# Performance work log

Hardware: AMD Instinct MI355X
Metric: run time of the kernel (lower is better)

The kernel has to match this reference:

```python
import jax, jax.numpy as jnp
from jax import lax
import numpy as np

# (pad, pool_kernel(h,w), pool_stride(h,w)) for each of the 7 conv layers
_CONV_CFG = [
    (1, (2, 2), (2, 2)),
    (1, (2, 2), (2, 2)),
    (1, (2, 2), (2, 1)),
    (1, (2, 2), (2, 1)),
    (1, (2, 2), (2, 2)),
    (1, (2, 2), (2, 1)),
    (0, (1, 1), (1, 1)),
]


def _conv_layer(x, w, b, pad, pool_k, pool_s):
    y = lax.conv_general_dilated(x, w, (1, 1), [(pad, pad), (pad, pad)],
                                 dimension_numbers=("NCHW", "OIHW", "NCHW"))
    y = jax.nn.relu(y + b[None, :, None, None])
    if pool_k != (1, 1):
        y = lax.reduce_window(y, -jnp.inf, lax.max, (1, 1) + pool_k, (1, 1) + pool_s, "VALID")
    return y


def _lstm_dir(x, wih, whh, bih, bhh, reverse):
    # x: [B,T,I]; PyTorch gate order i,f,g,o
    B = x.shape[0]
    H = whh.shape[1]
    xg = jnp.einsum("bti,gi->btg", x, wih) + bih + bhh  # [B,T,4H]

    def step(carry, xt):
        h, c = carry
        g = xt + h @ whh.T
        i, f, gg, o = jnp.split(g, 4, axis=-1)
        c = jax.nn.sigmoid(f) * c + jax.nn.sigmoid(i) * jnp.tanh(gg)
        h = jax.nn.sigmoid(o) * jnp.tanh(c)
        return (h, c), h

    init = (jnp.zeros((B, H), x.dtype), jnp.zeros((B, H), x.dtype))
    _, hs = lax.scan(step, init, jnp.swapaxes(xg, 0, 1), reverse=reverse)
    return jnp.swapaxes(hs, 0, 1)  # [B,T,H], time-ordered for both directions


def _bilstm2(x, wih, whh, bih, bhh, base):
    # 2-layer bidirectional LSTM; weight slots base..base+3 = (l0_fwd,l0_bwd,l1_fwd,l1_bwd)
    for l in range(2):
        i0 = base + 2 * l
        fwd = _lstm_dir(x, wih[i0], whh[i0], bih[i0], bhh[i0], False)
        bwd = _lstm_dir(x, wih[i0 + 1], whh[i0 + 1], bih[i0 + 1], bhh[i0 + 1], True)
        x = jnp.concatenate([fwd, bwd], axis=-1)
    return x


def _forward(x, conv_w0, conv_b0, conv_w1, conv_b1, conv_w2, conv_b2, conv_w3, conv_b3,
             conv_w4, conv_b4, conv_w5, conv_b5, conv_w6, conv_b6,
             lstm_wih, lstm_whh, lstm_bih, lstm_bhh,
             enc_proj_w, enc_proj_b, dec_proj_w, dec_proj_b, v_w,
             dec_wih, dec_whh, dec_bih, dec_bhh, dense_w, dense_b):
    conv_w = [conv_w0, conv_w1, conv_w2, conv_w3, conv_w4, conv_w5, conv_w6]
    conv_b = [conv_b0, conv_b1, conv_b2, conv_b3, conv_b4, conv_b5, conv_b6]
    y = x
    for i, (pad, pk, ps) in enumerate(_CONV_CFG):
        y = _conv_layer(y, conv_w[i], conv_b[i], pad, pk, ps)
    # y: [B,512,1,T] -> squeeze height, put time first-major: [B,T,512]
    y = jnp.transpose(y[:, :, 0, :], (0, 2, 1))
    seq = _bilstm2(y, lstm_wih, lstm_whh, lstm_bih, lstm_bhh, 0)
    seq = _bilstm2(seq, lstm_wih, lstm_whh, lstm_bih, lstm_bhh, 4)  # [B,T,512]

    # additive attention: enc projection is h-independent, precompute once
    enc = jnp.einsum("bte,ae->bta", seq, enc_proj_w) + enc_proj_b  # [B,T,256]
    B = x.shape[0]

    def dec_step(carry, _):
        h, c = carry
        dec = h @ dec_proj_w.T + dec_proj_b                      # [B,256]
        scores = jnp.tanh(enc + dec[:, None, :]) @ v_w[0]        # [B,T]
        aw = jax.nn.softmax(scores, axis=1)
        ctx = jnp.einsum("bt,bte->be", aw, seq)                  # [B,512]
        g = ctx @ dec_wih.T + dec_bih + h @ dec_whh.T + dec_bhh  # [B,2048]
        i, f, gg, o = jnp.split(g, 4, axis=-1)
        c = jax.nn.sigmoid(f) * c + jax.nn.sigmoid(i) * jnp.tanh(gg)
        h = jax.nn.sigmoid(o) * jnp.tanh(c)
        return (h, c), h @ dense_w.T + dense_b

    init = (jnp.zeros((B, 512), x.dtype), jnp.zeros((B, 512), x.dtype))
    _, outs = lax.scan(dec_step, init, None, length=25)  # [25,B,99] == permute(1,0,2)
    return outs


def setup_inputs() -> dict:
    key = jax.random.key(0)
    ks = jax.random.split(key, 32)

    def rn(i, shape, std):
        return jax.random.normal(ks[i], shape, jnp.float32) * std

    d = {"x": jax.random.normal(ks[0], (16, 1, 128, 512), jnp.float32)}
    chans = [(1, 64, 3), (64, 128, 3), (128, 256, 3), (256, 512, 3),
             (512, 512, 3), (512, 512, 3), (512, 512, 2)]
    for i, (ci, co, k) in enumerate(chans):
        d[f"conv_w{i}"] = rn(1 + i, (co, ci, k, k), (2.0 / (ci * k * k)) ** 0.5)
        d[f"conv_b{i}"] = rn(8 + i, (co,), 0.02)
    d["lstm_wih"] = rn(15, (8, 1024, 512), 0.06)
    d["lstm_whh"] = rn(16, (8, 1024, 256), 0.06)
    d["lstm_bih"] = rn(17, (8, 1024), 0.06)
    d["lstm_bhh"] = rn(18, (8, 1024), 0.06)
    d["enc_proj_w"] = rn(19, (256, 512), 0.04)
    d["enc_proj_b"] = rn(20, (256,), 0.02)
    d["dec_proj_w"] = rn(21, (256, 512), 0.04)
    d["dec_proj_b"] = rn(22, (256,), 0.02)
    d["v_w"] = rn(23, (1, 256), 0.06)
    d["dec_wih"] = rn(24, (2048, 512), 0.04)
    d["dec_whh"] = rn(25, (2048, 512), 0.04)
    d["dec_bih"] = rn(26, (2048,), 0.02)
    d["dec_bhh"] = rn(27, (2048,), 0.02)
    d["dense_w"] = rn(28, (99, 512), 0.04)
    d["dense_b"] = rn(29, (99,), 0.02)
    return d


def reference(x, conv_w0, conv_b0, conv_w1, conv_b1, conv_w2, conv_b2, conv_w3, conv_b3,
              conv_w4, conv_b4, conv_w5, conv_b5, conv_w6, conv_b6,
              lstm_wih, lstm_whh, lstm_bih, lstm_bhh,
              enc_proj_w, enc_proj_b, dec_proj_w, dec_proj_b, v_w,
              dec_wih, dec_whh, dec_bih, dec_bhh, dense_w, dense_b):
    return _forward(x, conv_w0, conv_b0, conv_w1, conv_b1, conv_w2, conv_b2, conv_w3, conv_b3,
                    conv_w4, conv_b4, conv_w5, conv_b5, conv_w6, conv_b6,
                    lstm_wih, lstm_whh, lstm_bih, lstm_bhh,
                    enc_proj_w, enc_proj_b, dec_proj_w, dec_proj_b, v_w,
                    dec_wih, dec_whh, dec_bih, dec_bhh, dense_w, dense_b)
```

## Files before the change

### kernel.cpp

```cpp
#include <hip/hip_runtime.h>
#include <math.h>

typedef short bf16x8 __attribute__((ext_vector_type(8)));
typedef float f32x4  __attribute__((ext_vector_type(4)));

__device__ __forceinline__ float sigmf(float x){ return 1.f/(1.f+expf(-x)); }
__device__ __forceinline__ short f2bf(float f){
    unsigned u = __float_as_uint(f);
    u = (u + 0x7FFFu + ((u>>16)&1u)) >> 16;
    return (short)u;
}
__device__ __forceinline__ float bf2f(short s){
    return __uint_as_float(((unsigned)(unsigned short)s) << 16);
}

__global__ void wsplit(const float* __restrict__ w, short* __restrict__ whi, short* __restrict__ wlo,
                       int Cout, int Cin, int KW, int total)
{
    int idx = blockIdx.x*256 + threadIdx.x;
    if (idx >= total) return;
    int l = idx & 63; int t = idx >> 6;
    int KST = Cin >> 5;
    int ks = t % KST; t /= KST;
    int nCoQ = Cout >> 4;
    int coQ = t % nCoQ; int kk = t / nCoQ;
    int ky = kk / KW, kx = kk % KW;
    int co = coQ*16 + (l & 15);
    int ci = ks*32 + (l >> 4)*8;
    bf16x8 h, lo;
#pragma unroll
    for (int e = 0; e < 8; ++e) {
        float wv = w[(((size_t)co*Cin + ci + e)*KW + ky)*KW + kx];
        short hb = f2bf(wv);
        h[e] = hb;
        lo[e] = f2bf(wv - bf2f(hb));
    }
    ((bf16x8*)whi)[idx] = h;
    ((bf16x8*)wlo)[idx] = lo;
}

template<int KW, int PKH, int PKW, int PSW, int PAD, bool FUSE0>
__launch_bounds__(256)
__global__ void conv_mfma(const float* __restrict__ in, const short* __restrict__ wm,
                          const float* __restrict__ bias, float* __restrict__ out,
                          int Cin, int H, int W, int Cout, int Hp, int Wp, int Wel,
                          const float* __restrict__ w0, const float* __restrict__ b0)
{
    constexpr int TAPS = KW*KW;
    constexpr int SR   = PKH + KW - 1;
    constexpr int XT   = 64;
    constexpr int XTH  = 67;
    constexpr int POB  = (XT - PKW)/PSW + 1;
    __shared__ union {
        short s[2][16][XTH][8];
        float y[64][132];
    } u;
    __shared__ float w0s[640];

    const int tid  = threadIdx.x;
    const int lane = tid & 63;
    const int wid  = tid >> 6;
    const int l15  = lane & 15, l4 = lane >> 4;
    const int nCoT = Cout >> 7;
    const int b    = blockIdx.z / nCoT;
    const int ct   = blockIdx.z % nCoT;
    const int co_blk = ct << 7;
    const int hp   = blockIdx.y;
    const int px0  = blockIdx.x * POB;
    const int x0   = px0 * PSW;
    const int y0   = hp * PKH;
    const int cow  = wid >> 1;
    const int xw   = (wid & 1) * 32;
    const int KST  = Cin >> 5;
    const int nCoQ = Cout >> 4;

    if constexpr (FUSE0) {
        for (int i = tid; i < 640; i += 256) w0s[i] = (i < 576) ? w0[i] : b0[i-576];
    }

    f32x4 acc[4][2][PKH];
#pragma unroll
    for (int c = 0; c < 4; ++c)
#pragma unroll
        for (int xf = 0; xf < 2; ++xf)
#pragma unroll
            for (int r = 0; r < PKH; ++r) acc[c][xf][r] = (f32x4){0.f,0.f,0.f,0.f};

    const float* inb = FUSE0 ? (in + (size_t)b*128*512) : (in + (size_t)b*H*W*Cin);

    for (int ci0 = 0; ci0 < Cin; ci0 += 32) {
        __syncthreads();
        constexpr int ITEMS = SR*XTH*4;
        for (int it = tid; it < ITEMS; it += 256) {
            int kslot = it & 3;
            int x  = (it >> 2) % XTH;
            int r  = (it >> 2) / XTH;
            int y  = y0 - PAD + r;
            int xg = x0 - PAD + x;
            float v[8];
            if constexpr (FUSE0) {
                if (y >= 0 && y < H && xg >= 0 && xg < W) {
                    float xin[4][4];
                    int iy0 = 2*y - 1, ix0 = 2*xg - 1;
#pragma unroll
                    for (int dy = 0; dy < 4; ++dy) {
                        int iy = iy0 + dy;
                        bool oky = (iy >= 0) && (iy < 128);
#pragma unroll
                        for (int dx = 0; dx < 4; ++dx) {
                            int ix = ix0 + dx;
                            xin[dy][dx] = (oky && ix >= 0 && ix < 512) ? inb[(size_t)iy*512 + ix] : 0.f;
                        }
                    }
#pragma unroll
                    for (int c = 0; c < 8; ++c) {
                        int co = ci0 + kslot*8 + c;
                        const float* w9 = &w0s[co*9];
                        float p00=0.f,p01=0.f,p10=0.f,p11=0.f;
#pragma unroll
                        for (int ky = 0; ky < 3; ++ky)
#pragma unroll
                            for (int kx = 0; kx < 3; ++kx) {
                                float wv = w9[ky*3+kx];
                                p00 = fmaf(xin[ky  ][kx  ], wv, p00);
                                p01 = fmaf(xin[ky  ][kx+1], wv, p01);
                                p10 = fmaf(xin[ky+1][kx  ], wv, p10);
                                p11 = fmaf(xin[ky+1][kx+1], wv, p11);
                            }
                        float m = fmaxf(fmaxf(p00,p01), fmaxf(p10,p11)) + w0s[576+co];
                        v[c] = fmaxf(m, 0.f);
                    }
                } else {
#pragma unroll
                    for (int c = 0; c < 8; ++c) v[c] = 0.f;
                }
            } else {
                if (y >= 0 && y < H && xg >= 0 && xg < W) {
                    const float* p = inb + ((size_t)y*W + xg)*Cin + ci0 + kslot*8;
                    float4 a = *(const float4*)p;
                    float4 bq = *(const float4*)(p+4);
                    v[0]=a.x; v[1]=a.y; v[2]=a.z; v[3]=a.w;
                    v[4]=bq.x; v[5]=bq.y; v[6]=bq.z; v[7]=bq.w;
                } else {
#pragma unroll
                    for (int c = 0; c < 8; ++c) v[c] = 0.f;
                }
            }
            bf16x8 h8, l8;
#pragma unroll
            for (int c = 0; c < 8; ++c) {
                short hb = f2bf(v[c]);
                h8[c] = hb;
                l8[c] = f2bf(v[c] - bf2f(hb));
            }
            *(bf16x8*)&u.s[0][r*4+kslot][x][0] = h8;
            *(bf16x8*)&u.s[1][r*4+kslot][x][0] = l8;
        }
        __syncthreads();

        const int ks = ci0 >> 5;
        for (int kk = 0; kk < TAPS; ++kk) {
            const int ky = kk / KW, kx = kk % KW;
            bf16x8 ah[4], al[4];
            const size_t abase = (((size_t)kk*nCoQ + (co_blk>>4) + cow*4)*KST + ks)*512 + lane*8;
            const size_t cstr  = (size_t)KST*512;
#pragma unroll
            for (int c = 0; c < 4; ++c) {
                ah[c] = *(const bf16x8*)(wm + abase + c*cstr);
                al[c] = *(const bf16x8*)(wm + Wel + abase + c*cstr);
            }
#pragma unroll
            for (int r = 0; r < PKH; ++r) {
                const int sr = r + ky;
                bf16x8 bh[2], bl[2];
#pragma unroll
                for (int xf = 0; xf < 2; ++xf) {
                    int xcol = xw + xf*16 + l15 + kx;
                    bh[xf] = *(const bf16x8*)&u.s[0][sr*4 + l4][xcol][0];
                    bl[xf] = *(const bf16x8*)&u.s[1][sr*4 + l4][xcol][0];
                }
#pragma unroll
                for (int c = 0; c < 4; ++c)
#pragma unroll
                    for (int xf = 0; xf < 2; ++xf) {
                        acc[c][xf][r] = __builtin_amdgcn_mfma_f32_16x16x32_bf16(ah[c], bh[xf], acc[c][xf][r], 0,0,0);
                        acc[c][xf][r] = __builtin_amdgcn_mfma_f32_16x16x32_bf16(ah[c], bl[xf], acc[c][xf][r], 0,0,0);
                        acc[c][xf][r] = __builtin_amdgcn_mfma_f32_16x16x32_bf16(al[c], bh[xf], acc[c][xf][r], 0,0,0);
                    }
            }
        }
    }

    __syncthreads();
#pragma unroll
    for (int c = 0; c < 4; ++c) {
        int co_l = cow*64 + c*16 + l4*4;
        float4 b4 = *(const float4*)&bias[co_blk + co_l];
#pragma unroll
        for (int xf = 0; xf < 2; ++xf) {
            f32x4 v = acc[c][xf][0];
            if (PKH == 2) {
                f32x4 v1 = acc[c][xf][1];
                v[0]=fmaxf(v[0],v1[0]); v[1]=fmaxf(v[1],v1[1]);
                v[2]=fmaxf(v[2],v1[2]); v[3]=fmaxf(v[3],v1[3]);
            }
            v[0]+=b4.x; v[1]+=b4.y; v[2]+=b4.z; v[3]+=b4.w;
            int x = xw + xf*16 + l15;
            *(f32x4*)&u.y[x][co_l] = v;
        }
    }
    __syncthreads();
    for (int i = tid; i < POB*128; i += 256) {
        int co = i & 127, p = i >> 7;
        int x = p * PSW;
        float v = u.y[x][co];
        if (PKW == 2) v = fmaxf(v, u.y[x+1][co]);
        v = fmaxf(v, 0.f);
        int px = px0 + p;
        if (px < Wp)
            out[(((size_t)b*Hp + hp)*Wp + px)*Cout + co_blk + co] = v;
    }
}

__launch_bounds__(256)
__global__ void gemm_nt(const float* __restrict__ A, const float* __restrict__ Bm,
                        const float* __restrict__ bias1, const float* __restrict__ bias2,
                        float* __restrict__ C, int M, int N, int K)
{
    __shared__ float As[16][68];
    __shared__ float Bs[16][68];
    const int tid = threadIdx.x;
    const int tx = tid & 15, ty = tid >> 4;
    const int row0 = blockIdx.y*64, col0 = blockIdx.x*64;
    float acc[4][4] = {};
    for (int k0 = 0; k0 < K; k0 += 16) {
#pragma unroll
        for (int i = 0; i < 4; ++i) {
            int e  = tid + i*256;
            int r  = e >> 4, kk = e & 15;
            int gr = row0 + r, gk = k0 + kk;
            As[kk][r] = (gr < M) ? A[(size_t)gr*K + gk] : 0.f;
            int gc = col0 + r;
            Bs[kk][r] = (gc < N) ? Bm[(size_t)gc*K + gk] : 0.f;
        }
        __syncthreads();
#pragma unroll
        for (int kk = 0; kk < 16; ++kk) {
            float av[4], bv[4];
#pragma unroll
            for (int i=0;i<4;++i) av[i] = As[kk][ty*4+i];
#pragma unroll
            for (int j=0;j<4;++j) bv[j] = Bs[kk][tx*4+j];
#pragma unroll
            for (int i=0;i<4;++i)
#pragma unroll
                for (int j=0;j<4;++j) acc[i][j] = fmaf(av[i], bv[j], acc[i][j]);
        }
        __syncthreads();
    }
#pragma unroll
    for (int i=0;i<4;++i)
#pragma unroll
        for (int j=0;j<4;++j) {
            int r = row0 + ty*4 + i, cc = col0 + tx*4 + j;
            if (r < M && cc < N) {
                float v = acc[i][j];
                if (bias1) v += bias1[cc];
                if (bias2) v += bias2[cc];
                C[(size_t)r*N + cc] = v;
            }
        }
}

__global__ void transpose2d(const float* __restrict__ in, float* __restrict__ out, int R, int C)
{
    int idx = blockIdx.x*256 + threadIdx.x;
    if (idx >= R*C) return;
    int r = idx / C, c = idx % C;
    out[(size_t)c*R + r] = in[idx];
}

__global__ void transpose_whh4(const float* __restrict__ in, float* __restrict__ out)
{
    int idx = blockIdx.x*256 + threadIdx.x;
    if (idx >= 8*1024*256) return;
    int l = idx / 262144, rem = idx % 262144;
    int g = rem >> 8, k = rem & 255;
    int j = g & 255, gate = g >> 8;
    out[(size_t)l*262144 + ((size_t)k*256 + j)*4 + gate] = in[idx];
}

__global__ void transpose_w4(const float* __restrict__ in, float* __restrict__ out)
{
    int idx = blockIdx.x*256 + threadIdx.x;
    if (idx >= 2048*512) return;
    int row = idx >> 9, k = idx & 511;
    int gate = row >> 9, j = row & 511;
    out[((size_t)k*512 + j)*4 + gate] = in[idx];
}

__launch_bounds__(1024)
__global__ void lstm_scan2(const float* __restrict__ xgf, const float* __restrict__ xgb,
                           const float* __restrict__ w4f, const float* __restrict__ w4b,
                           float* __restrict__ hout, int T)
{
    __shared__ float hs[256];
    __shared__ float part[4][256][4];
    const int b = blockIdx.x, dir = blockIdx.y;
    const int tid = threadIdx.x;
    const int j = tid & 255, ks = tid >> 8;
    const float* xg = dir ? xgb : xgf;
    const float4* w4 = (const float4*)(dir ? w4b : w4f);
    float c = 0.f;
    if (ks == 0) hs[j] = 0.f;
    __syncthreads();
    float* outp = hout + dir*256 + j;
    for (int s = 0; s < T; ++s) {
        int t = dir ? (T-1-s) : s;
        float a0=0.f,a1=0.f,a2=0.f,a3=0.f;
        const float4* wp = w4 + (size_t)(ks*64)*256 + j;
#pragma unroll 8
        for (int kk = 0; kk < 64; ++kk) {
            float hv = hs[ks*64 + kk];
            float4 w = wp[(size_t)kk*256];
            a0 = fmaf(hv, w.x, a0); a1 = fmaf(hv, w.y, a1);
            a2 = fmaf(hv, w.z, a2); a3 = fmaf(hv, w.w, a3);
        }
        part[ks][j][0]=a0; part[ks][j][1]=a1; part[ks][j][2]=a2; part[ks][j][3]=a3;
        __syncthreads();
        if (ks == 0) {
            const float* xr = xg + ((size_t)b*T + t)*1024;
            float gi = xr[j]     + part[0][j][0]+part[1][j][0]+part[2][j][0]+part[3][j][0];
            float gf = xr[256+j] + part[0][j][1]+part[1][j][1]+part[2][j][1]+part[3][j][1];
            float gg = xr[512+j] + part[0][j][2]+part[1][j][2]+part[2][j][2]+part[3][j][2];
            float go = xr[768+j] + part[0][j][3]+part[1][j][3]+part[2][j][3]+part[3][j][3];
            c = sigmf(gf)*c + sigmf(gi)*tanhf(gg);
            float h = sigmf(go)*tanhf(c);
            hs[j] = h;
            outp[((size_t)b*T + t)*512] = h;
        }
        __syncthreads();
    }
}

__global__ void zero_hc(float* __restrict__ h, float* __restrict__ c)
{
    int i = blockIdx.x*256 + threadIdx.x;
    if (i < 16*512) { h[i] = 0.f; c[i] = 0.f; }
}

__launch_bounds__(256)
__global__ void dec_att(const float* __restrict__ h, const float* __restrict__ seq,
                        const float* __restrict__ enc, const float* __restrict__ dpwT,
                        const float* __restrict__ dpb, const float* __restrict__ vw,
                        float* __restrict__ ctx, int T)
{
    __shared__ float hsm[512], dec[256], sc[64];
    const int b = blockIdx.x, tid = threadIdx.x;
    hsm[tid]     = h[b*512 + tid];
    hsm[256+tid] = h[b*512 + 256 + tid];
    __syncthreads();
    float s = dpb[tid];
    for (int k = 0; k < 512; ++k) s = fmaf(hsm[k], dpwT[(size_t)k*256 + tid], s);
    dec[tid] = s;
    __syncthreads();
    {
        int t = tid >> 2, sub = tid & 3;
        float p = 0.f;
        if (t < T) {
            const float* er = enc + ((size_t)b*T + t)*256 + sub*64;
            const float* dc = dec + sub*64;
            const float* vv = vw + sub*64;
            for (int a = 0; a < 64; ++a) p = fmaf(tanhf(er[a] + dc[a]), vv[a], p);
        }
        p += __shfl_xor(p, 1, 4); p += __shfl_xor(p, 2, 4);
        if (t < T && sub == 0) sc[t] = p;
    }
    __syncthreads();
    if (tid < 64) {
        float v = (tid < T) ? sc[tid] : -1e30f;
        float m = v;
        for (int o = 1; o < 64; o <<= 1) m = fmaxf(m, __shfl_xor(m, o, 64));
        float e = (tid < T) ? expf(v - m) : 0.f;
        float ssum = e;
        for (int o = 1; o < 64; o <<= 1) ssum += __shfl_xor(ssum, o, 64);
        if (tid < T) sc[tid] = e / ssum;
    }
    __syncthreads();
#pragma unroll
    for (int half = 0; half < 2; ++half) {
        int col = tid + half*256;
        float acc = 0.f;
        const float* sr = seq + (size_t)b*T*512 + col;
        for (int t = 0; t < T; ++t) acc = fmaf(sc[t], sr[(size_t)t*512], acc);
        ctx[b*512 + col] = acc;
    }
}

__launch_bounds__(256)
__global__ void gates_part(const float* __restrict__ ctx, const float* __restrict__ h,
                           const float* __restrict__ wi4, const float* __restrict__ wh4,
                           float* __restrict__ gpart)
{
    __shared__ float xs[16][128], hsh[16][128];
    const int jt = blockIdx.x, ks = blockIdx.y;
    const int tid = threadIdx.x;
    const int jl = tid & 127, bh = tid >> 7;
    const int j = jt*128 + jl;
    const int k0 = ks*128;
    for (int idx = tid; idx < 2048; idx += 256) {
        int bb = idx >> 7, kk = idx & 127;
        xs[bb][kk]  = ctx[bb*512 + k0 + kk];
        hsh[bb][kk] = h[bb*512 + k0 + kk];
    }
    __syncthreads();
    float acc[8][4];
#pragma unroll
    for (int bi=0;bi<8;++bi)
#pragma unroll
        for (int g=0;g<4;++g) acc[bi][g]=0.f;
    const float4* wip = (const float4*)wi4 + (size_t)k0*512 + j;
    const float4* whp = (const float4*)wh4 + (size_t)k0*512 + j;
#pragma unroll 2
    for (int kk = 0; kk < 128; ++kk) {
        float4 wa = wip[(size_t)kk*512];
        float4 wb = whp[(size_t)kk*512];
#pragma unroll
        for (int bi = 0; bi < 8; ++bi) {
            int bb = bh*8 + bi;
            float xv = xs[bb][kk], hv = hsh[bb][kk];
            acc[bi][0] = fmaf(xv, wa.x, fmaf(hv, wb.x, acc[bi][0]));
            acc[bi][1] = fmaf(xv, wa.y, fmaf(hv, wb.y, acc[bi][1]));
            acc[bi][2] = fmaf(xv, wa.z, fmaf(hv, wb.z, acc[bi][2]));
            acc[bi][3] = fmaf(xv, wa.w, fmaf(hv, wb.w, acc[bi][3]));
        }
    }
    float* gp = gpart + (size_t)ks*16*2048;
#pragma unroll
    for (int bi = 0; bi < 8; ++bi)
#pragma unroll
        for (int g = 0; g < 4; ++g)
            gp[(size_t)(bh*8+bi)*2048 + j*4 + g] = acc[bi][g];
}

__launch_bounds__(512)
__global__ void cell_dense(float* __restrict__ h, float* __restrict__ c,
                           const float* __restrict__ gpart,
                           const float* __restrict__ bih, const float* __restrict__ bhh,
                           const float* __restrict__ dwT, const float* __restrict__ dnb,
                           float* __restrict__ out)
{
    __shared__ float hsh[512];
    const int b = blockIdx.x, j = threadIdx.x;
    float gi = bih[j]        + bhh[j];
    float gf = bih[512+j]    + bhh[512+j];
    float gg = bih[1024+j]   + bhh[1024+j];
    float go = bih[1536+j]   + bhh[1536+j];
#pragma unroll
    for (int ks = 0; ks < 4; ++ks) {
        float4 gp = *(const float4*)(gpart + (size_t)ks*16*2048 + (size_t)b*2048 + j*4);
        gi += gp.x; gf += gp.y; gg += gp.z; go += gp.w;
    }
    float cn = sigmf(gf)*c[b*512+j] + sigmf(gi)*tanhf(gg);
    float hn = sigmf(go)*tanhf(cn);
    c[b*512+j] = cn; h[b*512+j] = hn; hsh[j] = hn;
    __syncthreads();
    int o = j >> 2, sub = j & 3;
    float p = 0.f;
    if (o < 99) {
        const float* hk = hsh + sub*128;
        const float* wk = dwT + (size_t)sub*128*99 + o;
        for (int k = 0; k < 128; ++k) p = fmaf(hk[k], wk[(size_t)k*99], p);
    }
    p += __shfl_xor(p, 1, 4); p += __shfl_xor(p, 2, 4);
    if (o < 99 && sub == 0) out[b*99 + o] = p + dnb[o];
}

extern "C" void kernel_launch(void* const* d_in, const int* in_sizes, int n_in,
                              void* d_out, int out_size, void* d_ws, size_t ws_size,
                              hipStream_t stream)
{
    (void)in_sizes; (void)n_in; (void)out_size; (void)ws_size;
    const float* x = (const float*)d_in[0];
    const float* convw[7]; const float* convb[7];
    for (int i = 0; i < 7; ++i) { convw[i] = (const float*)d_in[1+2*i]; convb[i] = (const float*)d_in[2+2*i]; }
    const float* lw   = (const float*)d_in[15];
    const float* lr   = (const float*)d_in[16];
    const float* lbi  = (const float*)d_in[17];
    const float* lbh  = (const float*)d_in[18];
    const float* encW = (const float*)d_in[19];
    const float* encB = (const float*)d_in[20];
    const float* dpw  = (const float*)d_in[21];
    const float* dpb  = (const float*)d_in[22];
    const float* vw   = (const float*)d_in[23];
    const float* dwih = (const float*)d_in[24];
    const float* dwhh = (const float*)d_in[25];
    const float* dbih = (const float*)d_in[26];
    const float* dbhh = (const float*)d_in[27];
    const float* dnw  = (const float*)d_in[28];
    const float* dnb  = (const float*)d_in[29];
    float* outp = (float*)d_out;

    float* ws    = (float*)d_ws;
    float* bufA  = ws;
    float* bufB  = ws + 8388608;
    float* wscr  = ws + 16777216;
    float* S0    = ws + 19136512;
    float* SY    = ws + 19636224;
    float* xg_f  = ws + 20135936;
    float* xg_b  = ws + 21135360;
    float* whhT4 = ws + 22134784;
    float* encb  = ws + 24231936;
    float* dpwT  = ws + 24481792;
    float* dwT   = ws + 24612864;
    float* hbuf  = ws + 24663552;
    float* cbuf  = ws + 24671744;
    float* ctxb  = ws + 24679936;
    float* gpart = ws + 24688128;
    float* wihT4 = bufA;
    float* whh2T4= bufB;

    short* whi = (short*)wscr;

    {
        int Wel = 9*(128/16)*(64/32)*512;
        wsplit<<<(Wel/8+255)/256, 256, 0, stream>>>(convw[1], whi, whi+Wel, 128, 64, 3, Wel/8);
        conv_mfma<3,2,2,2,1,true><<<dim3(4,32,16), 256, 0, stream>>>(
            x, whi, convb[1], bufA, 64,64,256,128, 32,128, Wel, convw[0], convb[0]);
    }
    {
        int Wel = 9*(256/16)*(128/32)*512;
        wsplit<<<(Wel/8+255)/256, 256, 0, stream>>>(convw[2], whi, whi+Wel, 256, 128, 3, Wel/8);
        conv_mfma<3,2,2,1,1,false><<<dim3(3,16,32), 256, 0, stream>>>(
            bufA, whi, convb[2], bufB, 128,32,128,256, 16,127, Wel, nullptr, nullptr);
    }
    {
        int Wel = 9*(512/16)*(256/32)*512;
        wsplit<<<(Wel/8+255)/256, 256, 0, stream>>>(convw[3], whi, whi+Wel, 512, 256, 3, Wel/8);
        conv_mfma<3,2,2,1,1,false><<<dim3(2,8,64), 256, 0, stream>>>(
            bufB, whi, convb[3], bufA, 256,16,127,512, 8,126, Wel, nullptr, nullptr);
    }
    {
        int Wel = 9*(512/16)*(512/32)*512;
        wsplit<<<(Wel/8+255)/256, 256, 0, stream>>>(convw[4], whi, whi+Wel, 512, 512, 3, Wel/8);
        conv_mfma<3,2,2,2,1,false><<<dim3(2,4,64), 256, 0, stream>>>(
            bufA, whi, convb[4], bufB, 512,8,126,512, 4,63, Wel, nullptr, nullptr);
    }
    {
        int Wel = 9*(512/16)*(512/32)*512;
        wsplit<<<(Wel/8+255)/256, 256, 0, stream>>>(convw[5], whi, whi+Wel, 512, 512, 3, Wel/8);
        conv_mfma<3,2,2,1,1,false><<<dim3(1,2,64), 256, 0, stream>>>(
            bufB, whi, convb[5], bufA, 512,4,63,512, 2,62, Wel, nullptr, nullptr);
    }
    {
        int Wel = 4*(512/16)*(512/32)*512;
        wsplit<<<(Wel/8+255)/256, 256, 0, stream>>>(convw[6], whi, whi+Wel, 512, 512, 2, Wel/8);
        conv_mfma<2,1,1,1,0,false><<<dim3(1,1,64), 256, 0, stream>>>(
            bufA, whi, convb[6], S0, 512,2,62,512, 1,61, Wel, nullptr, nullptr);
    }

    transpose_whh4<<<(8*1024*256 + 255)/256, 256, 0, stream>>>(lr, whhT4);
    transpose2d<<<(256*512 + 255)/256, 256, 0, stream>>>(dpw, dpwT, 256, 512);
    transpose_w4<<<(2048*512 + 255)/256, 256, 0, stream>>>(dwih, wihT4);
    transpose_w4<<<(2048*512 + 255)/256, 256, 0, stream>>>(dwhh, whh2T4);
    transpose2d<<<(99*512 + 255)/256, 256, 0, stream>>>(dnw, dwT, 99, 512);

    const int T = 61, M = 16*T;
    float* cur = S0; float* nxt = SY;
    for (int L = 0; L < 4; ++L) {
        int s0 = 2*L;
        gemm_nt<<<dim3(16, (M+63)/64), 256, 0, stream>>>(cur, lw + (size_t)s0*1024*512,
            lbi + s0*1024, lbh + s0*1024, xg_f, M, 1024, 512);
        gemm_nt<<<dim3(16, (M+63)/64), 256, 0, stream>>>(cur, lw + (size_t)(s0+1)*1024*512,
            lbi + (s0+1)*1024, lbh + (s0+1)*1024, xg_b, M, 1024, 512);
        lstm_scan2<<<dim3(16,2), 1024, 0, stream>>>(xg_f, xg_b,
            whhT4 + (size_t)s0*262144, whhT4 + (size_t)(s0+1)*262144, nxt, T);
        float* tmp = cur; cur = nxt; nxt = tmp;
    }

    gemm_nt<<<dim3(4, (M+63)/64), 256, 0, stream>>>(cur, encW, encB, nullptr, encb, M, 256, 512);

    zero_hc<<<32, 256, 0, stream>>>(hbuf, cbuf);
    for (int step = 0; step < 25; ++step) {
        dec_att<<<16, 256, 0, stream>>>(hbuf, cur, encb, dpwT, dpb, vw, ctxb, T);
        gates_part<<<dim3(4,4), 256, 0, stream>>>(ctxb, hbuf, wihT4, whh2T4, gpart);
        cell_dense<<<16, 512, 0, stream>>>(hbuf, cbuf, gpart, dbih, dbhh, dwT, dnb,
                                           outp + (size_t)step*16*99);
    }
}
```

Before: 5.371 ms.

## Use split-bf16 MFMA for LSTM input GEMMs and bf16 recurrent weights

Replaces the two fp32 SIMT input-projection GEMMs per LSTM layer with a single MFMA kernel that covers both directions. It uses a 3-term split-bf16 scheme (hi*hi + hi*lo + lo*hi) to keep close to fp32 accuracy. The recurrent weights in the scan kernel are stored as plain bf16, halving the weight bandwidth per timestep, and the xg gate loads are hoisted ahead of the matvec. Truncating the recurrent weights to bf16 lowers precision in the sequential scan, which may affect accuracy over 61 steps.

```diff
diff --git a/kernel.cpp b/kernel.cpp
--- a/kernel.cpp
+++ b/kernel.cpp
@@ -2,6 +2,7 @@
 #include <math.h>
 
 typedef short bf16x8 __attribute__((ext_vector_type(8)));
+typedef short s16x4  __attribute__((ext_vector_type(4)));
 typedef float f32x4  __attribute__((ext_vector_type(4)));
 
 __device__ __forceinline__ float sigmf(float x){ return 1.f/(1.f+expf(-x)); }
@@ -37,6 +38,28 @@
     }
     ((bf16x8*)whi)[idx] = h;
     ((bf16x8*)wlo)[idx] = lo;
+}
+
+__global__ void wsplit_g(const float* __restrict__ w, short* __restrict__ out)
+{
+    int slot = blockIdx.y;
+    int i = blockIdx.x*256 + threadIdx.x;
+    int l = i & 63, t = i >> 6;
+    int kc = t & 15, nQ = t >> 4;
+    int n = nQ*16 + (l & 15);
+    int k = kc*32 + (l >> 4)*8;
+    const float* src = w + ((size_t)slot*1024 + n)*512 + k;
+    bf16x8 h, lo;
+#pragma unroll
+    for (int e = 0; e < 8; ++e) {
+        float wv = src[e];
+        short hb = f2bf(wv);
+        h[e] = hb;
+        lo[e] = f2bf(wv - bf2f(hb));
+    }
+    short* o = out + (size_t)slot*1048576;
+    ((bf16x8*)o)[i] = h;
+    ((bf16x8*)(o + 524288))[i] = lo;
 }
 
 template<int KW, int PKH, int PKW, int PSW, int PAD, bool FUSE0>
@@ -223,6 +246,111 @@
 }
 
 __launch_bounds__(256)
+__global__ void gemm_mfma(const float* __restrict__ A, const short* __restrict__ wg,
+                          const float* __restrict__ bi, const float* __restrict__ bh,
+                          float* __restrict__ Cf, float* __restrict__ Cb,
+                          int M, int s0)
+{
+    __shared__ short sa[2][4][64][8];
+    const int tid = threadIdx.x;
+    const int lane = tid & 63;
+    const int wid = tid >> 6;
+    const int l15 = lane & 15, l4 = lane >> 4;
+    const int cow = wid >> 1;
+    const int xw  = wid & 1;
+    const int m0 = blockIdx.x * 64;
+    const int n0 = blockIdx.y * 128;
+    const int slot = s0 + blockIdx.z;
+    const short* whi = wg + (size_t)slot * 1048576;
+    const short* wlo = whi + 524288;
+    float* C = blockIdx.z ? Cb : Cf;
+    const float* b1 = bi + slot*1024;
+    const float* b2 = bh + slot*1024;
+
+    const int mg  = wid;
+    const int pos = tid & 63;
+    const int sm  = mg*16 + (pos & 15);
+    const int skl = pos >> 4;
+    const int gm  = m0 + sm;
+    const int nQb = blockIdx.y*8 + cow*4;
+
+    f32x4 acc[4][2];
+#pragma unroll
+    for (int c = 0; c < 4; ++c)
+#pragma unroll
+        for (int xf = 0; xf < 2; ++xf) acc[c][xf] = (f32x4){0.f,0.f,0.f,0.f};
+
+    for (int kc = 0; kc < 16; ++kc) {
+        __syncthreads();
+        {
+            float v[8];
+            if (gm < M) {
+                const float* ap = A + (size_t)gm*512 + kc*32 + skl*8;
+                float4 q0 = *(const float4*)ap;
+                float4 q1 = *(const float4*)(ap+4);
+                v[0]=q0.x; v[1]=q0.y; v[2]=q0.z; v[3]=q0.w;
+                v[4]=q1.x; v[5]=q1.y; v[6]=q1.z; v[7]=q1.w;
+            } else {
+#pragma unroll
+                for (int e = 0; e < 8; ++e) v[e] = 0.f;
+            }
+            bf16x8 h8, l8;
+#pragma unroll
+            for (int e = 0; e < 8; ++e) {
+                short hb = f2bf(v[e]);
+                h8[e] = hb;
+                l8[e] = f2bf(v[e] - bf2f(hb));
+            }
+            *(bf16x8*)&sa[0][mg][pos][0] = h8;
+            *(bf16x8*)&sa[1][mg][pos][0] = l8;
+        }
+        __syncthreads();
+
+        bf16x8 ah[4], al[4];
+#pragma unroll
+        for (int c = 0; c < 4; ++c) {
+            size_t off = (((size_t)(nQb + c)*16 + kc)*64 + lane)*8;
+            ah[c] = *(const bf16x8*)(whi + off);
+            al[c] = *(const bf16x8*)(wlo + off);
+        }
+        bf16x8 bhv[2], blv[2];
+#pragma unroll
+        for (int xf = 0; xf < 2; ++xf) {
+            bhv[xf] = *(const bf16x8*)&sa[0][xw*2+xf][lane][0];
+            blv[xf] = *(const bf16x8*)&sa[1][xw*2+xf][lane][0];
+        }
+#pragma unroll
+        for (int c = 0; c < 4; ++c)
+#pragma unroll
+            for (int xf = 0; xf < 2; ++xf) {
+                acc[c][xf] = __builtin_amdgcn_mfma_f32_16x16x32_bf16(ah[c], bhv[xf], acc[c][xf], 0,0,0);
+                acc[c][xf] = __builtin_amdgcn_mfma_f32_16x16x32_bf16(ah[c], blv[xf], acc[c][xf], 0,0,0);
+                acc[c][xf] = __builtin_amdgcn_mfma_f32_16x16x32_bf16(al[c], bhv[xf], acc[c][xf], 0,0,0);
+            }
+    }
+
+#pragma unroll
+    for (int c = 0; c < 4; ++c) {
+        int n = n0 + cow*64 + c*16 + l4*4;
+        float4 bb1 = *(const float4*)&b1[n];
+        float4 bb2 = *(const float4*)&b2[n];
+#pragma unroll
+        for (int xf = 0; xf < 2; ++xf) {
+            int m = m0 + xw*32 + xf*16 + l15;
+            if (m < M) {
+                f32x4 a = acc[c][xf];
+                float4 o;
+                o.x = a[0] + bb1.x + bb2.x;
+                o.y = a[1] + bb1.y + bb2.y;
+                o.z = a[2] + bb1.z + bb2.z;
+                o.w = a[3] + bb1.w + bb2.w;
+                *(float4*)&C[(size_t)m*1024 + n] = o;
+            }
+        }
+    }
+}
+
+__launch_bounds__(256)
 __global__ void gemm_nt(const float* __restrict__ A, const float* __restrict__ Bm,
                         const float* __restrict__ bias1, const float* __restrict__ bias2,
                         float* __restrict__ C, int M, int N, int K)
@@ -280,14 +408,14 @@
     out[(size_t)c*R + r] = in[idx];
 }
 
-__global__ void transpose_whh4(const float* __restrict__ in, float* __restrict__ out)
+__global__ void pack_whh_bf16(const float* __restrict__ in, short* __restrict__ out)
 {
     int idx = blockIdx.x*256 + threadIdx.x;
     if (idx >= 8*1024*256) return;
     int l = idx / 262144, rem = idx % 262144;
     int g = rem >> 8, k = rem & 255;
     int j = g & 255, gate = g >> 8;
-    out[(size_t)l*262144 + ((size_t)k*256 + j)*4 + gate] = in[idx];
+    out[(size_t)l*262144 + ((size_t)k*256 + j)*4 + gate] = f2bf(in[idx]);
 }
 
 __global__ void transpose_w4(const float* __restrict__ in, float* __restrict__ out)
@@ -300,8 +428,8 @@
 }
 
 __launch_bounds__(1024)
-__global__ void lstm_scan2(const float* __restrict__ xgf, const float* __restrict__ xgb,
-                           const float* __restrict__ w4f, const float* __restrict__ w4b,
+__global__ void lstm_scan3(const float* __restrict__ xgf, const float* __restrict__ xgb,
+                           const short* __restrict__ wBf, const short* __restrict__ wBb,
                            float* __restrict__ hout, int T)
 {
     __shared__ float hs[256];
@@ -310,30 +438,36 @@
     const int tid = threadIdx.x;
     const int j = tid & 255, ks = tid >> 8;
     const float* xg = dir ? xgb : xgf;
-    const float4* w4 = (const float4*)(dir ? w4b : w4f);
+    const s16x4* w4 = (const s16x4*)(dir ? wBb : wBf);
     float c = 0.f;
     if (ks == 0) hs[j] = 0.f;
     __syncthreads();
     float* outp = hout + dir*256 + j;
     for (int s = 0; s < T; ++s) {
         int t = dir ? (T-1-s) : s;
+        float xi=0.f, xf_=0.f, xg_=0.f, xo=0.f;
+        if (ks == 0) {
+            const float* xr = xg + ((size_t)b*T + t)*1024;
+            xi = xr[j]; xf_ = xr[256+j]; xg_ = xr[512+j]; xo = xr[768+j];
+        }
         float a0=0.f,a1=0.f,a2=0.f,a3=0.f;
-        const float4* wp = w4 + (size_t)(ks*64)*256 + j;
-#pragma unroll 8
+        const s16x4* wp = w4 + (size_t)(ks*64)*256 + j;
+#pragma unroll 16
         for (int kk = 0; kk < 64; ++kk) {
             float hv = hs[ks*64 + kk];
-            float4 w = wp[(size_t)kk*256];
-            a0 = fmaf(hv, w.x, a0); a1 = fmaf(hv, w.y, a1);
-            a2 = fmaf(hv, w.z, a2); a3 = fmaf(hv, w.w, a3);
+            s16x4 w = wp[(size_t)kk*256];
+            a0 = fmaf(hv, bf2f(w[0]), a0);
+            a1 = fmaf(hv, bf2f(w[1]), a1);
+            a2 = fmaf(hv, bf2f(w[2]), a2);
+            a3 = fmaf(hv, bf2f(w[3]), a3);
         }
         part[ks][j][0]=a0; part[ks][j][1]=a1; part[ks][j][2]=a2; part[ks][j][3]=a3;
         __syncthreads();
         if (ks == 0) {
-            const float* xr = xg + ((size_t)b*T + t)*1024;
-            float gi = xr[j]     + part[0][j][0]+part[1][j][0]+part[2][j][0]+part[3][j][0];
-            float gf = xr[256+j] + part[0][j][1]+part[1][j][1]+part[2][j][1]+part[3][j][1];
-            float gg = xr[512+j] + part[0][j][2]+part[1][j][2]+part[2][j][2]+part[3][j][2];
-            float go = xr[768+j] + part[0][j][3]+part[1][j][3]+part[2][j][3]+part[3][j][3];
+            float gi = xi  + part[0][j][0]+part[1][j][0]+part[2][j][0]+part[3][j][0];
+            float gf = xf_ + part[0][j][1]+part[1][j][1]+part[2][j][1]+part[3][j][1];
+            float gg = xg_ + part[0][j][2]+part[1][j][2]+part[2][j][2]+part[3][j][2];
+            float go = xo  + part[0][j][3]+part[1][j][3]+part[2][j][3]+part[3][j][3];
             c = sigmf(gf)*c + sigmf(gi)*tanhf(gg);
             float h = sigmf(go)*tanhf(c);
             hs[j] = h;
@@ -509,7 +643,7 @@
     float* SY    = ws + 19636224;
     float* xg_f  = ws + 20135936;
     float* xg_b  = ws + 21135360;
-    float* whhT4 = ws + 22134784;
+    float* whhBf = ws + 22134784;
     float* encb  = ws + 24231936;
     float* dpwT  = ws + 24481792;
     float* dwT   = ws + 24612864;
@@ -519,6 +653,8 @@
     float* gpart = ws + 24688128;
     float* wihT4 = bufA;
     float* whh2T4= bufB;
+    short* wgB   = (short*)(bufA + 1048576);
+    short* whhB  = (short*)whhBf;
 
     short* whi = (short*)wscr;
 
@@ -559,7 +695,8 @@
             bufA, whi, convb[6], S0, 512,2,62,512, 1,61, Wel, nullptr, nullptr);
     }
 
-    transpose_whh4<<<(8*1024*256 + 255)/256, 256, 0, stream>>>(lr, whhT4);
+    wsplit_g<<<dim3(256, 8), 256, 0, stream>>>(lw, wgB);
+    pack_whh_bf16<<<(8*1024*256 + 255)/256, 256, 0, stream>>>(lr, whhB);
     transpose2d<<<(256*512 + 255)/256, 256, 0, stream>>>(dpw, dpwT, 256, 512);
     transpose_w4<<<(2048*512 + 255)/256, 256, 0, stream>>>(dwih, wihT4);
     transpose_w4<<<(2048*512 + 255)/256, 256, 0, stream>>>(dwhh, whh2T4);
@@ -569,12 +706,9 @@
     float* cur = S0; float* nxt = SY;
     for (int L = 0; L < 4; ++L) {
         int s0 = 2*L;
-        gemm_nt<<<dim3(16, (M+63)/64), 256, 0, stream>>>(cur, lw + (size_t)s0*1024*512,
-            lbi + s0*1024, lbh + s0*1024, xg_f, M, 1024, 512);
-        gemm_nt<<<dim3(16, (M+63)/64), 256, 0, stream>>>(cur, lw + (size_t)(s0+1)*1024*512,
-            lbi + (s0+1)*1024, lbh + (s0+1)*1024, xg_b, M, 1024, 512);
-        lstm_scan2<<<dim3(16,2), 1024, 0, stream>>>(xg_f, xg_b,
-            whhT4 + (size_t)s0*262144, whhT4 + (size_t)(s0+1)*262144, nxt, T);
+        gemm_mfma<<<dim3(16, 8, 2), 256, 0, stream>>>(cur, wgB, lbi, lbh, xg_f, xg_b, M, s0);
+        lstm_scan3<<<dim3(16,2), 1024, 0, stream>>>(xg_f, xg_b,
+            whhB + (size_t)s0*262144, whhB + (size_t)(s0+1)*262144, nxt, T);
         float* tmp = cur; cur = nxt; nxt = tmp;
     }
 
```

Result: faster. 5.081 ms (-5.4%).
